# Kernel tuning notes

Hardware: AMD Instinct MI355X
Metric: run time of the kernel (lower is better)

Reference implementation:

```python
import jax, jax.numpy as jnp
import numpy as np

N = 50000   # nodes
E = 800000  # edges
D = 128     # input feature dim
H = 128     # hidden_channels
O = 128     # out_channels
NEG_SLOPE = 0.2


def setup_inputs() -> dict:
    key = jax.random.key(0)
    ks = jax.random.split(key, 16)
    x = jax.random.normal(ks[0], (N, D), dtype=jnp.float32)
    edge_idx = jax.random.randint(ks[1], (2, E), 0, N, dtype=jnp.int32)

    def lin(k, fin, fout):
        return jax.random.normal(k, (fin, fout), dtype=jnp.float32) / np.sqrt(fin)

    params = {
        # layer 1 (D -> H)
        "Wl1": lin(ks[2], D, H), "bl1": jnp.zeros((H,), jnp.float32),
        "Wr1": lin(ks[3], D, H), "br1": jnp.zeros((H,), jnp.float32),
        "att1": jax.random.normal(ks[4], (H,), dtype=jnp.float32) / np.sqrt(H),
        "b1": jnp.zeros((H,), jnp.float32),
        # layer 2 (H -> O)
        "Wl2": lin(ks[5], H, O), "bl2": jnp.zeros((O,), jnp.float32),
        "Wr2": lin(ks[6], H, O), "br2": jnp.zeros((O,), jnp.float32),
        "att2": jax.random.normal(ks[7], (O,), dtype=jnp.float32) / np.sqrt(O),
        "b2": jnp.zeros((O,), jnp.float32),
    }
    return {"x": x, "edge_idx": edge_idx, **params}


def gatv2_layer(x, src, dst, Wl, bl, Wr, br, att, bias):
    """Single-head GATv2Conv (add_self_loops=False), PyG semantics.

    message(x_j) uses lin_l(x_j); score uses leaky_relu(lin_l(x_j)+lin_r(x_i)) @ att,
    softmax over in-edges of each target node, scatter-add weighted messages.
    """
    xl = x @ Wl + bl            # [N, F] source transform
    xr = x @ Wr + br            # [N, F] target transform
    msg = xl[src]               # [E, F] gathered source messages
    e = jax.nn.leaky_relu(msg + xr[dst], NEG_SLOPE)  # [E, F]
    s = e @ att                 # [E] unnormalized scores
    smax = jax.lax.stop_gradient(jax.ops.segment_max(s, dst, num_segments=N))
    p = jnp.exp(s - smax[dst])  # stable segment softmax numerator
    denom = jax.ops.segment_sum(p, dst, num_segments=N)  # [N]
    alpha = p / denom[dst]      # [E]
    out = jax.ops.segment_sum(alpha[:, None] * msg, dst, num_segments=N)
    return out + bias


def reference(x, edge_idx, Wl1, bl1, Wr1, br1, att1, b1, Wl2, bl2, Wr2, br2, att2, b2):
    src, dst = edge_idx[0], edge_idx[1]
    h = jax.nn.relu(gatv2_layer(x, src, dst, Wl1, bl1, Wr1, br1, att1, b1))
    out = gatv2_layer(h, src, dst, Wl2, bl2, Wr2, br2, att2, b2)
    return out
```

## Files before the change

### kernel.cpp

```cpp
#include <hip/hip_runtime.h>
#include <math.h>


typedef short bf16x8 __attribute__((ext_vector_type(8)));
typedef float f32x4 __attribute__((ext_vector_type(4)));

__global__ __launch_bounds__(256) void count_prep_kernel(
    const int* __restrict__ dst, int* __restrict__ deg8,
    unsigned short* __restrict__ rank16, int E, int N, int nCnt,
    const float* __restrict__ W0, const float* __restrict__ W1,
    const float* __restrict__ W2, const float* __restrict__ W3,
    short* __restrict__ wt) {
    if ((int)blockIdx.x < nCnt) {
        int i = blockIdx.x * 256 + threadIdx.x;
        if (i < E) {
            int slice = blockIdx.x & 7;
            int r = atomicAdd(&deg8[(size_t)slice * N + dst[i]], 1);
            rank16[i] = (unsigned short)r;
        }
    } else {
        int b = blockIdx.x - nCnt;
        int mat = b >> 3, chunk = b & 7;
        const float* W = (mat == 0) ? W0 : (mat == 1) ? W1 : (mat == 2) ? W2 : W3;
        short* hi = wt + (size_t)mat * 2 * 16384;
        short* lo = hi + 16384;
        int i0 = chunk * 2048;
        for (int i = i0 + threadIdx.x; i < i0 + 2048; i += 256) {
            int k = i >> 7, n = i & 127;
            float x = W[i];
            unsigned u = __float_as_uint(x);
            unsigned hu = u & 0xFFFF0000u;
            float lf = x - __uint_as_float(hu);
            hi[n * 128 + k] = (short)(hu >> 16);
            lo[n * 128 + k] = (short)(__float_as_uint(lf) >> 16);
        }
    }
}

__global__ __launch_bounds__(256) void scan_blocksum2_kernel(
    const int* __restrict__ deg8, unsigned short* __restrict__ base8,
    int* __restrict__ dtot, int* __restrict__ blockSums, int n) {
    __shared__ int wsum[4];
    int tid = threadIdx.x;
    int idx = blockIdx.x * 256 + tid;
    int lane = tid & 63, wid = tid >> 6;
    int tot = 0;
    if (idx < n) {
        int b = 0;
        #pragma unroll
        for (int s = 0; s < 8; ++s) {
            int v = deg8[(size_t)s * n + idx];
            base8[(size_t)s * n + idx] = (unsigned short)b;
            b += v;
        }
        tot = b;
        dtot[idx] = tot;
    }
    int v = tot;
    #pragma unroll
    for (int off = 32; off > 0; off >>= 1) v += __shfl_xor(v, off);
    if (lane == 0) wsum[wid] = v;
    __syncthreads();
    if (tid == 0) blockSums[blockIdx.x] = wsum[0] + wsum[1] + wsum[2] + wsum[3];
}

__global__ __launch_bounds__(256) void scan_apply2_kernel(
    const int* __restrict__ dtot, const int* __restrict__ blockSums,
    const unsigned short* __restrict__ base8,
    int* __restrict__ row_ptr, int* __restrict__ rpb, int n, int nBlk) {
    __shared__ int sPre[4], sAll[4], wsum[4];
    int tid = threadIdx.x, lane = tid & 63, wid = tid >> 6;

    int bsv = (tid < nBlk) ? blockSums[tid] : 0;
    int pre = (tid < (int)blockIdx.x) ? bsv : 0;
    int all = bsv;
    #pragma unroll
    for (int off = 32; off > 0; off >>= 1) {
        pre += __shfl_xor(pre, off);
        all += __shfl_xor(all, off);
    }
    if (lane == 0) { sPre[wid] = pre; sAll[wid] = all; }
    __syncthreads();
    int off0 = sPre[0] + sPre[1] + sPre[2] + sPre[3];
    int total = sAll[0] + sAll[1] + sAll[2] + sAll[3];

    int idx = blockIdx.x * 256 + tid;
    int v = (idx < n) ? dtot[idx] : 0;
    int incl = v;
    #pragma unroll
    for (int off = 1; off < 64; off <<= 1) {
        int t = __shfl_up(incl, off);
        if (lane >= off) incl += t;
    }
    if (lane == 63) wsum[wid] = incl;
    __syncthreads();
    int woff = 0;
    #pragma unroll
    for (int w = 0; w < 4; ++w) woff += (w < wid) ? wsum[w] : 0;
    int excl = off0 + woff + (incl - v);
    if (idx < n) {
        row_ptr[idx] = excl;
        #pragma unroll
        for (int s = 0; s < 8; ++s)
            rpb[(size_t)s * n + idx] = excl + (int)base8[(size_t)s * n + idx];
    }
    if (blockIdx.x == 0 && tid == 0) row_ptr[n] = total;
}

__global__ void scatter_edges_kernel(const int* __restrict__ src, const int* __restrict__ dst,
                                     const int* __restrict__ rpb,
                                     const unsigned short* __restrict__ rank16,
                                     unsigned short* __restrict__ csr16, int E, int N) {
    int i = blockIdx.x * blockDim.x + threadIdx.x;
    if (i < E) {
        int d = dst[i];
        int slice = blockIdx.x & 7;
        int pos = rpb[(size_t)slice * N + d] + (int)rank16[i];
        csr16[pos] = (unsigned short)src[i];
    }
}

#define LDK 136
__global__ __launch_bounds__(256) void gemm_mfma_dual32_kernel(
    const float* __restrict__ X, const short* __restrict__ wtL,
    const float* __restrict__ b0, short* __restrict__ out0bf,
    const float* __restrict__ b1, float* __restrict__ out1,
    int Nrows) {
    __shared__ __attribute__((aligned(16))) short Ahi[32][LDK];
    __shared__ __attribute__((aligned(16))) short Alo[32][LDK];

    int tid = threadIdx.x;
    int w = tid >> 6, lane = tid & 63, q = lane >> 4, tr = lane & 15;
    int m0 = blockIdx.x * 32;
    int n0 = w * 32;

    bf16x8 bh[4], bl[4];
    #pragma unroll
    for (int p = 0; p < 2; ++p) {
        const short* base = wtL + (size_t)p * 2 * 16384;
        #pragma unroll
        for (int nt = 0; nt < 2; ++nt) {
            size_t boff = (size_t)(n0 + nt * 16 + tr) * 128 + q * 8;
            bh[p * 2 + nt] = *(const bf16x8*)&base[boff];
            bl[p * 2 + nt] = *(const bf16x8*)&base[16384 + boff];
        }
    }

    {
        int srow = tid >> 3;
        int c0 = (tid & 7) * 16;
        int gr = m0 + srow; if (gr >= Nrows) gr = Nrows - 1;
        const float* xp = &X[(size_t)gr * 128 + c0];
        float4 v[4];
        #pragma unroll
        for (int j = 0; j < 4; ++j) v[j] = *(const float4*)(xp + j * 4);
        #pragma unroll
        for (int j = 0; j < 2; ++j) {
            bf16x8 hv, lv;
            #pragma unroll
            for (int k = 0; k < 2; ++k) {
                float4 vv = v[j * 2 + k];
                float f[4] = {vv.x, vv.y, vv.z, vv.w};
                #pragma unroll
                for (int e = 0; e < 4; ++e) {
                    unsigned u = __float_as_uint(f[e]);
                    unsigned hu = u & 0xFFFF0000u;
                    float lf = f[e] - __uint_as_float(hu);
                    hv[k * 4 + e] = (short)(hu >> 16);
                    lv[k * 4 + e] = (short)(__float_as_uint(lf) >> 16);
                }
            }
            *(bf16x8*)&Ahi[srow][c0 + j * 8] = hv;
            *(bf16x8*)&Alo[srow][c0 + j * 8] = lv;
        }
    }
    __syncthreads();

    f32x4 acc[2][4];
    #pragma unroll
    for (int a = 0; a < 2; ++a)
        #pragma unroll
        for (int b = 0; b < 4; ++b) acc[a][b] = (f32x4){0.f, 0.f, 0.f, 0.f};

    for (int kc = 0; kc < 128; kc += 32) {
        #pragma unroll
        for (int mt = 0; mt < 2; ++mt) {
            bf16x8 ah = *(const bf16x8*)&Ahi[mt * 16 + tr][kc + q * 8];
            bf16x8 al = *(const bf16x8*)&Alo[mt * 16 + tr][kc + q * 8];
            #pragma unroll
            for (int j = 0; j < 4; ++j) {
                acc[mt][j] = __builtin_amdgcn_mfma_f32_16x16x32_bf16(ah, bh[j], acc[mt][j], 0, 0, 0);
                acc[mt][j] = __builtin_amdgcn_mfma_f32_16x16x32_bf16(ah, bl[j], acc[mt][j], 0, 0, 0);
                acc[mt][j] = __builtin_amdgcn_mfma_f32_16x16x32_bf16(al, bh[j], acc[mt][j], 0, 0, 0);
            }
        }
        if (kc < 96) {
            #pragma unroll
            for (int p = 0; p < 2; ++p) {
                const short* base = wtL + (size_t)p * 2 * 16384;
                #pragma unroll
                for (int nt = 0; nt < 2; ++nt) {
                    size_t boff = (size_t)(n0 + nt * 16 + tr) * 128 + (kc + 32) + q * 8;
                    bh[p * 2 + nt] = *(const bf16x8*)&base[boff];
                    bl[p * 2 + nt] = *(const bf16x8*)&base[16384 + boff];
                }
            }
        }
    }

    #pragma unroll
    for (int nt = 0; nt < 2; ++nt) {
        float bv0 = b0[n0 + nt * 16 + tr];
        float bv1 = b1[n0 + nt * 16 + tr];
        #pragma unroll
        for (int mt = 0; mt < 2; ++mt) {
            #pragma unroll
            for (int r = 0; r < 4; ++r) {
                int row = m0 + mt * 16 + q * 4 + r;
                if (row < Nrows) {
                    float v0 = acc[mt][nt][r] + bv0;
                    unsigned u = __float_as_uint(v0);
                    unsigned rb = (u + 0x7FFFu + ((u >> 16) & 1u)) >> 16;
                    out0bf[(size_t)row * 128 + n0 + nt * 16 + tr] = (short)rb;
                    out1[(size_t)row * 128 + n0 + nt * 16 + tr] = acc[mt][2 + nt][r] + bv1;
                }
            }
        }
    }
}
#undef LDK

__global__ __launch_bounds__(256) void gat_aggregate_kernel(
    const short* __restrict__ xl16, const float* __restrict__ xr,
    const float* __restrict__ att, const float* __restrict__ bias,
    const int* __restrict__ row_ptr, const unsigned short* __restrict__ csr16,
    float* __restrict__ out, int N, int applyRelu) {
    int wid = threadIdx.x >> 6;
    int lane = threadIdx.x & 63;
    int qlane = lane & 15;
    int qid = lane >> 4;
    int node = blockIdx.x * 4 + wid;
    if (node >= N) return;

    const bf16x8* xlb = (const bf16x8*)xl16;
    float4 xrA = ((const float4*)xr)[(size_t)node * 32 + qlane * 2];
    float4 xrB = ((const float4*)xr)[(size_t)node * 32 + qlane * 2 + 1];
    float4 atA = ((const float4*)att)[qlane * 2];
    float4 atB = ((const float4*)att)[qlane * 2 + 1];

    int beg = row_ptr[node];
    int end = row_ptr[node + 1];

    float dsum = 0.f;
    float4 accA = {0.f, 0.f, 0.f, 0.f};
    float4 accB = {0.f, 0.f, 0.f, 0.f};

    for (int cbase = beg; cbase < end; cbase += 64) {
        int cnt = end - cbase;
        if (cnt > 64) cnt = 64;
        int myidx = (lane < cnt) ? (int)csr16[cbase + lane] : 0;
        int nq = (cnt + 3) >> 2;

        for (int g = 0; g < nq; ++g) {
            int eidx = 4 * g + qid;
            int s = __shfl(myidx, eidx);
            bf16x8 mv = xlb[((size_t)s << 4) + qlane];
            float4 vA, vB;
            vA.x = __uint_as_float(((unsigned)(unsigned short)mv[0]) << 16);
            vA.y = __uint_as_float(((unsigned)(unsigned short)mv[1]) << 16);
            vA.z = __uint_as_float(((unsigned)(unsigned short)mv[2]) << 16);
            vA.w = __uint_as_float(((unsigned)(unsigned short)mv[3]) << 16);
            vB.x = __uint_as_float(((unsigned)(unsigned short)mv[4]) << 16);
            vB.y = __uint_as_float(((unsigned)(unsigned short)mv[5]) << 16);
            vB.z = __uint_as_float(((unsigned)(unsigned short)mv[6]) << 16);
            vB.w = __uint_as_float(((unsigned)(unsigned short)mv[7]) << 16);

            float t, p;
            t = vA.x + xrA.x; t = fmaxf(t, 0.2f * t); p = t * atA.x;
            t = vA.y + xrA.y; t = fmaxf(t, 0.2f * t); p = fmaf(t, atA.y, p);
            t = vA.z + xrA.z; t = fmaxf(t, 0.2f * t); p = fmaf(t, atA.z, p);
            t = vA.w + xrA.w; t = fmaxf(t, 0.2f * t); p = fmaf(t, atA.w, p);
            t = vB.x + xrB.x; t = fmaxf(t, 0.2f * t); p = fmaf(t, atB.x, p);
            t = vB.y + xrB.y; t = fmaxf(t, 0.2f * t); p = fmaf(t, atB.y, p);
            t = vB.z + xrB.z; t = fmaxf(t, 0.2f * t); p = fmaf(t, atB.z, p);
            t = vB.w + xrB.w; t = fmaxf(t, 0.2f * t); p = fmaf(t, atB.w, p);

            p += __shfl_xor(p, 1);
            p += __shfl_xor(p, 2);
            p += __shfl_xor(p, 4);
            p += __shfl_xor(p, 8);

            float e = (eidx < cnt) ? __expf(p) : 0.f;
            dsum += e;
            accA.x = fmaf(e, vA.x, accA.x);
            accA.y = fmaf(e, vA.y, accA.y);
            accA.z = fmaf(e, vA.z, accA.z);
            accA.w = fmaf(e, vA.w, accA.w);
            accB.x = fmaf(e, vB.x, accB.x);
            accB.y = fmaf(e, vB.y, accB.y);
            accB.z = fmaf(e, vB.z, accB.z);
            accB.w = fmaf(e, vB.w, accB.w);
        }
    }

    #pragma unroll
    for (int off = 16; off <= 32; off <<= 1) {
        dsum += __shfl_xor(dsum, off);
        accA.x += __shfl_xor(accA.x, off);
        accA.y += __shfl_xor(accA.y, off);
        accA.z += __shfl_xor(accA.z, off);
        accA.w += __shfl_xor(accA.w, off);
        accB.x += __shfl_xor(accB.x, off);
        accB.y += __shfl_xor(accB.y, off);
        accB.z += __shfl_xor(accB.z, off);
        accB.w += __shfl_xor(accB.w, off);
    }

    float inv = dsum > 0.f ? 1.f / dsum : 0.f;
    float4 bvA = ((const float4*)bias)[qlane * 2];
    float4 bvB = ((const float4*)bias)[qlane * 2 + 1];
    float4 oA, oB;
    oA.x = accA.x * inv + bvA.x; oA.y = accA.y * inv + bvA.y;
    oA.z = accA.z * inv + bvA.z; oA.w = accA.w * inv + bvA.w;
    oB.x = accB.x * inv + bvB.x; oB.y = accB.y * inv + bvB.y;
    oB.z = accB.z * inv + bvB.z; oB.w = accB.w * inv + bvB.w;
    if (applyRelu) {
        oA.x = fmaxf(oA.x, 0.f); oA.y = fmaxf(oA.y, 0.f);
        oA.z = fmaxf(oA.z, 0.f); oA.w = fmaxf(oA.w, 0.f);
        oB.x = fmaxf(oB.x, 0.f); oB.y = fmaxf(oB.y, 0.f);
        oB.z = fmaxf(oB.z, 0.f); oB.w = fmaxf(oB.w, 0.f);
    }
    if (lane < 16) {
        ((float4*)out)[(size_t)node * 32 + qlane * 2] = oA;
        ((float4*)out)[(size_t)node * 32 + qlane * 2 + 1] = oB;
    }
}


extern "C" void kernel_launch(void* const* d_in, const int* in_sizes, int n_in,
                              void* d_out, int out_size, void* d_ws, size_t ws_size,
                              hipStream_t stream) {
    const float* x    = (const float*)d_in[0];
    const int* eidx   = (const int*)d_in[1];
    const float* Wl1  = (const float*)d_in[2];
    const float* bl1  = (const float*)d_in[3];
    const float* Wr1  = (const float*)d_in[4];
    const float* br1  = (const float*)d_in[5];
    const float* att1 = (const float*)d_in[6];
    const float* b1   = (const float*)d_in[7];
    const float* Wl2  = (const float*)d_in[8];
    const float* bl2  = (const float*)d_in[9];
    const float* Wr2  = (const float*)d_in[10];
    const float* br2  = (const float*)d_in[11];
    const float* att2 = (const float*)d_in[12];
    const float* b2   = (const float*)d_in[13];

    const int N = in_sizes[0] / 128;
    const int E = in_sizes[1] / 2;
    const int* src = eidx;
    const int* dst = eidx + E;

    const int nBlk = (N + 255) / 256;

    size_t NF = (size_t)N * 128;
    short* xl16 = (short*)d_ws;
    float* bufB = (float*)(xl16 + NF);
    float* bufC = bufB + NF;
    int* deg8      = (int*)(bufC + NF);
    int* dtot      = deg8 + 8 * (size_t)N;
    int* row_ptr   = dtot + N;
    int* blockSums = row_ptr + (N + 1);
    int* rpb       = blockSums + nBlk;
    unsigned short* base8  = (unsigned short*)(rpb + 8 * (size_t)N);
    unsigned short* rank16 = base8 + 8 * (size_t)N;
    unsigned short* csr16  = rank16 + E;
    short* wt      = (short*)(csr16 + E);

    float* outF = (float*)d_out;

    const int nCnt = (E + 255) / 256;
    hipMemsetAsync(deg8, 0, 8 * (size_t)N * sizeof(int), stream);
    count_prep_kernel<<<nCnt + 32, 256, 0, stream>>>(dst, deg8, rank16, E, N, nCnt,
                                                     Wl1, Wr1, Wl2, Wr2, wt);
    scan_blocksum2_kernel<<<nBlk, 256, 0, stream>>>(deg8, base8, dtot, blockSums, N);
    scan_apply2_kernel<<<nBlk, 256, 0, stream>>>(dtot, blockSums, base8, row_ptr, rpb, N, nBlk);
    scatter_edges_kernel<<<nCnt, 256, 0, stream>>>(src, dst, rpb, rank16, csr16, E, N);

    dim3 gemmGrid((N + 31) / 32);
    dim3 aggGrid((N + 3) / 4);

    gemm_mfma_dual32_kernel<<<gemmGrid, 256, 0, stream>>>(x, wt, bl1, xl16, br1, bufB, N);
    gat_aggregate_kernel<<<aggGrid, 256, 0, stream>>>(xl16, bufB, att1, b1, row_ptr, csr16,
                                                      bufC, N, 1);
    gemm_mfma_dual32_kernel<<<gemmGrid, 256, 0, stream>>>(bufC, wt + 2 * 2 * 16384, bl2, xl16,
                                                          br2, bufB, N);
    gat_aggregate_kernel<<<aggGrid, 256, 0, stream>>>(xl16, bufB, att2, b2, row_ptr, csr16,
                                                      outF, N, 0);
}
```

Baseline: 296.7 us.

## Fuse degree counting into layer-1 GEMM launch and zero counters in prep kernel

Replaces the memset plus count/prep launch with a small prep kernel that zeroes the per-slice degree counters and splits the weights. The edge degree-count atomics are then folded into the layer-1 GEMM launch as extra blocks, so counting and the first GEMM run concurrently. The slice index now derives from the edge index rather than the block id so count and scatter stay consistent. This removes a launch and a memset and overlaps atomic-heavy counting with MFMA work. The GEMM blocks in that combined launch all reserve the shared-memory tiles, including the count blocks that never use them.

```diff
diff --git a/kernel.cpp b/kernel.cpp
--- a/kernel.cpp
+++ b/kernel.cpp
@@ -5,133 +5,38 @@
 typedef short bf16x8 __attribute__((ext_vector_type(8)));
 typedef float f32x4 __attribute__((ext_vector_type(4)));
 
-__global__ __launch_bounds__(256) void count_prep_kernel(
-    const int* __restrict__ dst, int* __restrict__ deg8,
-    unsigned short* __restrict__ rank16, int E, int N, int nCnt,
+#define LDK 136
+
+__global__ __launch_bounds__(256) void prep_zero_kernel(
     const float* __restrict__ W0, const float* __restrict__ W1,
     const float* __restrict__ W2, const float* __restrict__ W3,
-    short* __restrict__ wt) {
-    if ((int)blockIdx.x < nCnt) {
-        int i = blockIdx.x * 256 + threadIdx.x;
-        if (i < E) {
-            int slice = blockIdx.x & 7;
-            int r = atomicAdd(&deg8[(size_t)slice * N + dst[i]], 1);
-            rank16[i] = (unsigned short)r;
-        }
-    } else {
-        int b = blockIdx.x - nCnt;
-        int mat = b >> 3, chunk = b & 7;
-        const float* W = (mat == 0) ? W0 : (mat == 1) ? W1 : (mat == 2) ? W2 : W3;
-        short* hi = wt + (size_t)mat * 2 * 16384;
-        short* lo = hi + 16384;
-        int i0 = chunk * 2048;
-        for (int i = i0 + threadIdx.x; i < i0 + 2048; i += 256) {
-            int k = i >> 7, n = i & 127;
-            float x = W[i];
-            unsigned u = __float_as_uint(x);
-            unsigned hu = u & 0xFFFF0000u;
-            float lf = x - __uint_as_float(hu);
-            hi[n * 128 + k] = (short)(hu >> 16);
-            lo[n * 128 + k] = (short)(__float_as_uint(lf) >> 16);
-        }
-    }
-}
-
-__global__ __launch_bounds__(256) void scan_blocksum2_kernel(
-    const int* __restrict__ deg8, unsigned short* __restrict__ base8,
-    int* __restrict__ dtot, int* __restrict__ blockSums, int n) {
-    __shared__ int wsum[4];
-    int tid = threadIdx.x;
-    int idx = blockIdx.x * 256 + tid;
-    int lane = tid & 63, wid = tid >> 6;
-    int tot = 0;
-    if (idx < n) {
-        int b = 0;
-        #pragma unroll
-        for (int s = 0; s < 8; ++s) {
-            int v = deg8[(size_t)s * n + idx];
-            base8[(size_t)s * n + idx] = (unsigned short)b;
-            b += v;
-        }
-        tot = b;
-        dtot[idx] = tot;
-    }
-    int v = tot;
-    #pragma unroll
-    for (int off = 32; off > 0; off >>= 1) v += __shfl_xor(v, off);
-    if (lane == 0) wsum[wid] = v;
-    __syncthreads();
-    if (tid == 0) blockSums[blockIdx.x] = wsum[0] + wsum[1] + wsum[2] + wsum[3];
-}
-
-__global__ __launch_bounds__(256) void scan_apply2_kernel(
-    const int* __restrict__ dtot, const int* __restrict__ blockSums,
-    const unsigned short* __restrict__ base8,
-    int* __restrict__ row_ptr, int* __restrict__ rpb, int n, int nBlk) {
-    __shared__ int sPre[4], sAll[4], wsum[4];
-    int tid = threadIdx.x, lane = tid & 63, wid = tid >> 6;
-
-    int bsv = (tid < nBlk) ? blockSums[tid] : 0;
-    int pre = (tid < (int)blockIdx.x) ? bsv : 0;
-    int all = bsv;
-    #pragma unroll
-    for (int off = 32; off > 0; off >>= 1) {
-        pre += __shfl_xor(pre, off);
-        all += __shfl_xor(all, off);
-    }
-    if (lane == 0) { sPre[wid] = pre; sAll[wid] = all; }
-    __syncthreads();
-    int off0 = sPre[0] + sPre[1] + sPre[2] + sPre[3];
-    int total = sAll[0] + sAll[1] + sAll[2] + sAll[3];
-
-    int idx = blockIdx.x * 256 + tid;
-    int v = (idx < n) ? dtot[idx] : 0;
-    int incl = v;
-    #pragma unroll
-    for (int off = 1; off < 64; off <<= 1) {
-        int t = __shfl_up(incl, off);
-        if (lane >= off) incl += t;
-    }
-    if (lane == 63) wsum[wid] = incl;
-    __syncthreads();
-    int woff = 0;
-    #pragma unroll
-    for (int w = 0; w < 4; ++w) woff += (w < wid) ? wsum[w] : 0;
-    int excl = off0 + woff + (incl - v);
-    if (idx < n) {
-        row_ptr[idx] = excl;
-        #pragma unroll
-        for (int s = 0; s < 8; ++s)
-            rpb[(size_t)s * n + idx] = excl + (int)base8[(size_t)s * n + idx];
-    }
-    if (blockIdx.x == 0 && tid == 0) row_ptr[n] = total;
-}
-
-__global__ void scatter_edges_kernel(const int* __restrict__ src, const int* __restrict__ dst,
-                                     const int* __restrict__ rpb,
-                                     const unsigned short* __restrict__ rank16,
-                                     unsigned short* __restrict__ csr16, int E, int N) {
-    int i = blockIdx.x * blockDim.x + threadIdx.x;
-    if (i < E) {
-        int d = dst[i];
-        int slice = blockIdx.x & 7;
-        int pos = rpb[(size_t)slice * N + d] + (int)rank16[i];
-        csr16[pos] = (unsigned short)src[i];
-    }
-}
-
-#define LDK 136
-__global__ __launch_bounds__(256) void gemm_mfma_dual32_kernel(
-    const float* __restrict__ X, const short* __restrict__ wtL,
+    short* __restrict__ wt, int* __restrict__ deg8, int total8N) {
+    int b = blockIdx.x;
+    for (int j = b * 256 + threadIdx.x; j < total8N; j += 32 * 256) deg8[j] = 0;
+    int mat = b >> 3, chunk = b & 7;
+    const float* W = (mat == 0) ? W0 : (mat == 1) ? W1 : (mat == 2) ? W2 : W3;
+    short* hi = wt + (size_t)mat * 2 * 16384;
+    short* lo = hi + 16384;
+    int i0 = chunk * 2048;
+    for (int i = i0 + threadIdx.x; i < i0 + 2048; i += 256) {
+        int k = i >> 7, n = i & 127;
+        float x = W[i];
+        unsigned u = __float_as_uint(x);
+        unsigned hu = u & 0xFFFF0000u;
+        float lf = x - __uint_as_float(hu);
+        hi[n * 128 + k] = (short)(hu >> 16);
+        lo[n * 128 + k] = (short)(__float_as_uint(lf) >> 16);
+    }
+}
+
+__device__ __forceinline__ void gemm_dual32_body(
+    int bx, const float* __restrict__ X, const short* __restrict__ wtL,
     const float* __restrict__ b0, short* __restrict__ out0bf,
     const float* __restrict__ b1, float* __restrict__ out1,
-    int Nrows) {
-    __shared__ __attribute__((aligned(16))) short Ahi[32][LDK];
-    __shared__ __attribute__((aligned(16))) short Alo[32][LDK];
-
+    int Nrows, short (&Ahi)[32][LDK], short (&Alo)[32][LDK]) {
     int tid = threadIdx.x;
     int w = tid >> 6, lane = tid & 63, q = lane >> 4, tr = lane & 15;
-    int m0 = blockIdx.x * 32;
+    int m0 = bx * 32;
     int n0 = w * 32;
 
     bf16x8 bh[4], bl[4];
@@ -228,7 +133,119 @@
         }
     }
 }
-#undef LDK
+
+__global__ __launch_bounds__(256) void gemm_mfma_dual32_kernel(
+    const float* __restrict__ X, const short* __restrict__ wtL,
+    const float* __restrict__ b0, short* __restrict__ out0bf,
+    const float* __restrict__ b1, float* __restrict__ out1, int Nrows) {
+    __shared__ __attribute__((aligned(16))) short Ahi[32][LDK];
+    __shared__ __attribute__((aligned(16))) short Alo[32][LDK];
+    gemm_dual32_body(blockIdx.x, X, wtL, b0, out0bf, b1, out1, Nrows, Ahi, Alo);
+}
+
+__global__ __launch_bounds__(256) void gemm1_count_kernel(
+    const float* __restrict__ X, const short* __restrict__ wtL,
+    const float* __restrict__ b0, short* __restrict__ out0bf,
+    const float* __restrict__ b1, float* __restrict__ out1,
+    int Nrows, int gemmBlocks,
+    const int* __restrict__ dst, int* __restrict__ deg8,
+    unsigned short* __restrict__ rank16, int E, int N) {
+    __shared__ __attribute__((aligned(16))) short Ahi[32][LDK];
+    __shared__ __attribute__((aligned(16))) short Alo[32][LDK];
+    if ((int)blockIdx.x < gemmBlocks) {
+        gemm_dual32_body(blockIdx.x, X, wtL, b0, out0bf, b1, out1, Nrows, Ahi, Alo);
+    } else {
+        int i = (blockIdx.x - gemmBlocks) * 256 + threadIdx.x;
+        if (i < E) {
+            int slice = (i >> 8) & 7;
+            int r = atomicAdd(&deg8[(size_t)slice * N + dst[i]], 1);
+            rank16[i] = (unsigned short)r;
+        }
+    }
+}
+
+__global__ __launch_bounds__(256) void scan_blocksum2_kernel(
+    const int* __restrict__ deg8, unsigned short* __restrict__ base8,
+    int* __restrict__ dtot, int* __restrict__ blockSums, int n) {
+    __shared__ int wsum[4];
+    int tid = threadIdx.x;
+    int idx = blockIdx.x * 256 + tid;
+    int lane = tid & 63, wid = tid >> 6;
+    int tot = 0;
+    if (idx < n) {
+        int b = 0;
+        #pragma unroll
+        for (int s = 0; s < 8; ++s) {
+            int v = deg8[(size_t)s * n + idx];
+            base8[(size_t)s * n + idx] = (unsigned short)b;
+            b += v;
+        }
+        tot = b;
+        dtot[idx] = tot;
+    }
+    int v = tot;
+    #pragma unroll
+    for (int off = 32; off > 0; off >>= 1) v += __shfl_xor(v, off);
+    if (lane == 0) wsum[wid] = v;
+    __syncthreads();
+    if (tid == 0) blockSums[blockIdx.x] = wsum[0] + wsum[1] + wsum[2] + wsum[3];
+}
+
+__global__ __launch_bounds__(256) void scan_apply2_kernel(
+    const int* __restrict__ dtot, const int* __restrict__ blockSums,
+    const unsigned short* __restrict__ base8,
+    int* __restrict__ row_ptr, int* __restrict__ rpb, int n, int nBlk) {
+    __shared__ int sPre[4], sAll[4], wsum[4];
+    int tid = threadIdx.x, lane = tid & 63, wid = tid >> 6;
+
+    int bsv = (tid < nBlk) ? blockSums[tid] : 0;
+    int pre = (tid < (int)blockIdx.x) ? bsv : 0;
+    int all = bsv;
+    #pragma unroll
+    for (int off = 32; off > 0; off >>= 1) {
+        pre += __shfl_xor(pre, off);
+        all += __shfl_xor(all, off);
+    }
+    if (lane == 0) { sPre[wid] = pre; sAll[wid] = all; }
+    __syncthreads();
+    int off0 = sPre[0] + sPre[1] + sPre[2] + sPre[3];
+    int total = sAll[0] + sAll[1] + sAll[2] + sAll[3];
+
+    int idx = blockIdx.x * 256 + tid;
+    int v = (idx < n) ? dtot[idx] : 0;
+    int incl = v;
+    #pragma unroll
+    for (int off = 1; off < 64; off <<= 1) {
+        int t = __shfl_up(incl, off);
+        if (lane >= off) incl += t;
+    }
+    if (lane == 63) wsum[wid] = incl;
+    __syncthreads();
+    int woff = 0;
+    #pragma unroll
+    for (int w = 0; w < 4; ++w) woff += (w < wid) ? wsum[w] : 0;
+    int excl = off0 + woff + (incl - v);
+    if (idx < n) {
+        row_ptr[idx] = excl;
+        #pragma unroll
+        for (int s = 0; s < 8; ++s)
+            rpb[(size_t)s * n + idx] = excl + (int)base8[(size_t)s * n + idx];
+    }
+    if (blockIdx.x == 0 && tid == 0) row_ptr[n] = total;
+}
+
+__global__ void scatter_edges_kernel(const int* __restrict__ src, const int* __restrict__ dst,
+                                     const int* __restrict__ rpb,
+                                     const unsigned short* __restrict__ rank16,
+                                     unsigned short* __restrict__ csr16, int E, int N) {
+    int i = blockIdx.x * blockDim.x + threadIdx.x;
+    if (i < E) {
+        int d = dst[i];
+        int slice = (i >> 8) & 7;
+        int pos = rpb[(size_t)slice * N + d] + (int)rank16[i];
+        csr16[pos] = (unsigned short)src[i];
+    }
+}
 
 __global__ __launch_bounds__(256) void gat_aggregate_kernel(
     const short* __restrict__ xl16, const float* __restrict__ xr,
@@ -379,21 +396,19 @@
     float* outF = (float*)d_out;
 
     const int nCnt = (E + 255) / 256;
-    hipMemsetAsync(deg8, 0, 8 * (size_t)N * sizeof(int), stream);
-    count_prep_kernel<<<nCnt + 32, 256, 0, stream>>>(dst, deg8, rank16, E, N, nCnt,
-                                                     Wl1, Wr1, Wl2, Wr2, wt);
+    const int gemmBlocks = (N + 31) / 32;
+    dim3 aggGrid((N + 3) / 4);
+
+    prep_zero_kernel<<<32, 256, 0, stream>>>(Wl1, Wr1, Wl2, Wr2, wt, deg8, 8 * N);
+    gemm1_count_kernel<<<gemmBlocks + nCnt, 256, 0, stream>>>(
+        x, wt, bl1, xl16, br1, bufB, N, gemmBlocks, dst, deg8, rank16, E, N);
     scan_blocksum2_kernel<<<nBlk, 256, 0, stream>>>(deg8, base8, dtot, blockSums, N);
     scan_apply2_kernel<<<nBlk, 256, 0, stream>>>(dtot, blockSums, base8, row_ptr, rpb, N, nBlk);
     scatter_edges_kernel<<<nCnt, 256, 0, stream>>>(src, dst, rpb, rank16, csr16, E, N);
-
-    dim3 gemmGrid((N + 31) / 32);
-    dim3 aggGrid((N + 3) / 4);
-
-    gemm_mfma_dual32_kernel<<<gemmGrid, 256, 0, stream>>>(x, wt, bl1, xl16, br1, bufB, N);
     gat_aggregate_kernel<<<aggGrid, 256, 0, stream>>>(xl16, bufB, att1, b1, row_ptr, csr16,
                                                       bufC, N, 1);
-    gemm_mfma_dual32_kernel<<<gemmGrid, 256, 0, stream>>>(bufC, wt + 2 * 2 * 16384, bl2, xl16,
-                                                          br2, bufB, N);
+    gemm_mfma_dual32_kernel<<<gemmBlocks, 256, 0, stream>>>(bufC, wt + 2 * 2 * 16384, bl2, xl16,
+                                                            br2, bufB, N);
     gat_aggregate_kernel<<<aggGrid, 256, 0, stream>>>(xl16, bufB, att2, b2, row_ptr, csr16,
                                                       outF, N, 0);
 }
```

Result: no change. 294.3 us (-0.8%).
